# Performance work log

Measured on AMD Instinct MI355X. Metric: run time of the kernel, lower is better.

The kernel has to match this reference:

```python
import jax, jax.numpy as jnp
import numpy as np

B, N, C, H = 8, 1024, 768, 12
D = C // H  # head_dim = 64
SCALE = D ** -0.5
EPS = 1e-5  # nn.LayerNorm default


def layer_norm(x, gamma, beta):
    # normalize over last dim (head_dim)
    mu = jnp.mean(x, axis=-1, keepdims=True)
    var = jnp.var(x, axis=-1, keepdims=True)
    return (x - mu) * jax.lax.rsqrt(var + EPS) * gamma + beta


def setup_inputs() -> dict:
    key = jax.random.key(0)
    ks = jax.random.split(key, 5)
    s = 0.02
    return {
        "x": jax.random.normal(ks[0], (B, N, C), jnp.float32),
        "qkv_w": jax.random.normal(ks[1], (3 * C, C), jnp.float32) * s,
        "qkv_b": jax.random.normal(ks[2], (3 * C,), jnp.float32) * s,
        "q_gamma": jnp.ones((D,), jnp.float32),
        "q_beta": jnp.zeros((D,), jnp.float32),
        "k_gamma": jnp.ones((D,), jnp.float32),
        "k_beta": jnp.zeros((D,), jnp.float32),
        "proj_w": jax.random.normal(ks[3], (C, C), jnp.float32) * s,
        "proj_b": jax.random.normal(ks[4], (C,), jnp.float32) * s,
    }


def reference(x, qkv_w, qkv_b, q_gamma, q_beta, k_gamma, k_beta, proj_w, proj_b):
    Bx, Nx, Cx = x.shape
    qkv = x @ qkv_w.T + qkv_b                       # [B,N,3C]
    qkv = qkv.reshape(Bx, Nx, 3, H, D).transpose(2, 0, 3, 1, 4)  # [3,B,H,N,D]
    q, k, v = qkv[0], qkv[1], qkv[2]
    q = layer_norm(q, q_gamma, q_beta) * SCALE
    k = layer_norm(k, k_gamma, k_beta)
    attn = jax.nn.softmax(jnp.einsum('bhnd,bhmd->bhnm', q, k), axis=-1)  # [B,H,N,N]
    # attn_drop is identity (p=0, eval)
    out = jnp.einsum('bhnm,bhmd->bhnd', attn, v)    # [B,H,N,D]
    out = out.transpose(0, 2, 1, 3).reshape(Bx, Nx, Cx)
    out = out @ proj_w.T + proj_b                   # proj_drop identity
    return out, attn
```

## Files before the change

### kernel.cpp

```cpp
#include <hip/hip_runtime.h>
#include <hip/hip_bf16.h>
#include <stdint.h>

typedef __bf16 bf16_t;
typedef __bf16 bf16x8 __attribute__((ext_vector_type(8)));
typedef __bf16 bf16x4 __attribute__((ext_vector_type(4)));
typedef float f32x4 __attribute__((ext_vector_type(4)));

#define DEV static __device__ __forceinline__

DEV f32x4 mfma16(bf16x8 a, bf16x8 b, f32x4 c) {
  return __builtin_amdgcn_mfma_f32_16x16x32_bf16(a, b, c, 0, 0, 0);
}

DEV void gll16(const void* g, void* l) {
  __builtin_amdgcn_global_load_lds(
      (const __attribute__((address_space(1))) uint32_t*)g,
      (__attribute__((address_space(3))) uint32_t*)l, 16, 0, 0);
}

DEV int swz128(int row, int c16) {
  return (row << 7) + (((c16 ^ row) & 7) << 4);
}
DEV int swzel128(int row, int col) {
  return (row << 7) + ((((col >> 3) ^ row) & 7) << 4) + ((col & 7) << 1);
}

DEV void stage_tile_gll(const bf16_t* g, long rstride, char* lds, int wave, int lane) {
  int r0 = wave * 8 + (lane >> 3);
  int b = lane & 7;
#pragma unroll
  for (int q = 0; q < 2; q++) {
    int row = q * 32 + r0;
    gll16(g + (long)row * rstride + (((b ^ row) & 7) << 3),
          lds + q * 4096 + wave * 1024);
  }
}

__global__ void __launch_bounds__(256)
cast_all(const float* __restrict__ x, bf16_t* __restrict__ ox,
         const float* __restrict__ w1, bf16_t* __restrict__ ow1,
         const float* __restrict__ w2, bf16_t* __restrict__ ow2) {
  long i = (long)(blockIdx.x * 256 + threadIdx.x) * 8;
  const float* s; bf16_t* d; long off;
  if (i < 6291456L)      { s = x;  d = ox;  off = i; }
  else if (i < 8060928L) { s = w1; d = ow1; off = i - 6291456L; }
  else if (i < 8650752L) { s = w2; d = ow2; off = i - 8060928L; }
  else return;
  float4 a = *(const float4*)(s + off);
  float4 b = *(const float4*)(s + off + 4);
  bf16x8 v;
  v[0] = (bf16_t)a.x; v[1] = (bf16_t)a.y; v[2] = (bf16_t)a.z; v[3] = (bf16_t)a.w;
  v[4] = (bf16_t)b.x; v[5] = (bf16_t)b.y; v[6] = (bf16_t)b.z; v[7] = (bf16_t)b.w;
  *(bf16x8*)(d + off) = v;
}

#define C1Q 0.1803368801111244f

__global__ void __launch_bounds__(256, 2)
gemm_qkv_ln(const bf16_t* __restrict__ A, const bf16_t* __restrict__ Bw,
            const float* __restrict__ bias,
            const float* __restrict__ qg, const float* __restrict__ qb,
            const float* __restrict__ kg, const float* __restrict__ kb,
            bf16_t* __restrict__ qkv, int M, int N, int K) {
  __shared__ __align__(16) char As[8192];
  __shared__ __align__(16) char Bs[8192];
  const int tid = threadIdx.x;
  const int lane = tid & 63;
  const int wave = tid >> 6;
  const int wr = wave >> 1, wc = wave & 1;
  const int tileM = blockIdx.y << 7;
  const int tileN = blockIdx.x << 7;
  const int lrow = lane & 15, lk = lane >> 4;

  f32x4 acc[4][4];
  f32x4 z = {0.f, 0.f, 0.f, 0.f};
#pragma unroll
  for (int m = 0; m < 4; m++)
#pragma unroll
    for (int n = 0; n < 4; n++) acc[m][n] = z;

  const int srow = wave * 16 + (lane >> 2);
  const int sb = lane & 3;
  const bf16_t* Asrc0 = A + (long)(tileM + srow) * K + sb * 8;
  const bf16_t* Asrc1 = A + (long)(tileM + 64 + srow) * K + sb * 8;
  const bf16_t* Bsrc0 = Bw + (long)(tileN + srow) * K + sb * 8;
  const bf16_t* Bsrc1 = Bw + (long)(tileN + 64 + srow) * K + sb * 8;
  char* Adst = As + wave * 1024;
  char* Bdst = Bs + wave * 1024;

  for (int k0 = 0; k0 < K; k0 += 32) {
    __syncthreads();
    gll16(Asrc0 + k0, Adst);
    gll16(Asrc1 + k0, Adst + 4096);
    gll16(Bsrc0 + k0, Bdst);
    gll16(Bsrc1 + k0, Bdst + 4096);
    __syncthreads();
    bf16x8 af[4], bfr[4];
#pragma unroll
    for (int m = 0; m < 4; m++)
      af[m] = *(const bf16x8*)(As + (wr * 64 + m * 16 + lrow) * 64 + lk * 16);
#pragma unroll
    for (int n = 0; n < 4; n++)
      bfr[n] = *(const bf16x8*)(Bs + (wc * 64 + n * 16 + lrow) * 64 + lk * 16);
#pragma unroll
    for (int m = 0; m < 4; m++)
#pragma unroll
      for (int n = 0; n < 4; n++)
        acc[m][n] = mfma16(af[m], bfr[n], acc[m][n]);
  }

  const int t = tileN / 768;
  const int cbase = tileN + wc * 64;
  float g[4], be[4], bv[4];
#pragma unroll
  for (int n = 0; n < 4; n++) bv[n] = bias[cbase + n * 16 + lrow];
  if (t == 0) {
#pragma unroll
    for (int n = 0; n < 4; n++) {
      int d = n * 16 + lrow;
      g[n] = qg[d] * C1Q; be[n] = qb[d] * C1Q;
    }
  } else if (t == 1) {
#pragma unroll
    for (int n = 0; n < 4; n++) {
      int d = n * 16 + lrow;
      g[n] = kg[d]; be[n] = kb[d];
    }
  }

#pragma unroll
  for (int m = 0; m < 4; m++) {
#pragma unroll
    for (int r = 0; r < 4; r++) {
      float v[4];
#pragma unroll
      for (int n = 0; n < 4; n++) v[n] = acc[m][n][r] + bv[n];
      long row = tileM + wr * 64 + m * 16 + lk * 4 + r;
      bf16_t* dst = qkv + row * 2304 + cbase;
      if (t < 2) {
        float s = v[0] + v[1] + v[2] + v[3];
        float s2 = v[0]*v[0] + v[1]*v[1] + v[2]*v[2] + v[3]*v[3];
#pragma unroll
        for (int ofs = 1; ofs <= 8; ofs <<= 1) {
          s  += __shfl_xor(s, ofs);
          s2 += __shfl_xor(s2, ofs);
        }
        float mu = s * (1.f / 64.f);
        float rstd = rsqrtf(s2 * (1.f / 64.f) - mu * mu + 1e-5f);
#pragma unroll
        for (int n = 0; n < 4; n++)
          dst[n * 16 + lrow] = (bf16_t)((v[n] - mu) * rstd * g[n] + be[n]);
      } else {
#pragma unroll
        for (int n = 0; n < 4; n++)
          dst[n * 16 + lrow] = (bf16_t)v[n];
      }
    }
  }
}

__global__ void __launch_bounds__(256, 2)
gemm_bt(const bf16_t* __restrict__ A, const bf16_t* __restrict__ Bw,
        const float* __restrict__ bias, float* __restrict__ Cout,
        int M, int N, int K) {
  __shared__ __align__(16) char As[8192];
  __shared__ __align__(16) char Bs[8192];
  const int tid = threadIdx.x;
  const int lane = tid & 63;
  const int wave = tid >> 6;
  const int wr = wave >> 1, wc = wave & 1;
  const int tileM = blockIdx.y << 7;
  const int tileN = blockIdx.x << 7;
  const int lrow = lane & 15, lk = lane >> 4;

  f32x4 acc[4][4];
  f32x4 z = {0.f, 0.f, 0.f, 0.f};
#pragma unroll
  for (int m = 0; m < 4; m++)
#pragma unroll
    for (int n = 0; n < 4; n++) acc[m][n] = z;

  const int srow = wave * 16 + (lane >> 2);
  const int sb = lane & 3;
  const bf16_t* Asrc0 = A + (long)(tileM + srow) * K + sb * 8;
  const bf16_t* Asrc1 = A + (long)(tileM + 64 + srow) * K + sb * 8;
  const bf16_t* Bsrc0 = Bw + (long)(tileN + srow) * K + sb * 8;
  const bf16_t* Bsrc1 = Bw + (long)(tileN + 64 + srow) * K + sb * 8;
  char* Adst = As + wave * 1024;
  char* Bdst = Bs + wave * 1024;

  for (int k0 = 0; k0 < K; k0 += 32) {
    __syncthreads();
    gll16(Asrc0 + k0, Adst);
    gll16(Asrc1 + k0, Adst + 4096);
    gll16(Bsrc0 + k0, Bdst);
    gll16(Bsrc1 + k0, Bdst + 4096);
    __syncthreads();
    bf16x8 af[4], bfr[4];
#pragma unroll
    for (int m = 0; m < 4; m++)
      af[m] = *(const bf16x8*)(As + (wr * 64 + m * 16 + lrow) * 64 + lk * 16);
#pragma unroll
    for (int n = 0; n < 4; n++)
      bfr[n] = *(const bf16x8*)(Bs + (wc * 64 + n * 16 + lrow) * 64 + lk * 16);
#pragma unroll
    for (int m = 0; m < 4; m++)
#pragma unroll
      for (int n = 0; n < 4; n++)
        acc[m][n] = mfma16(af[m], bfr[n], acc[m][n]);
  }

  const int rg = lk;
#pragma unroll
  for (int n = 0; n < 4; n++) {
    int col = tileN + wc * 64 + n * 16 + lrow;
    float bv = bias[col];
#pragma unroll
    for (int m = 0; m < 4; m++) {
      long row0 = tileM + wr * 64 + m * 16 + rg * 4;
#pragma unroll
      for (int r = 0; r < 4; r++)
        Cout[(row0 + r) * N + col] = acc[m][n][r] + bv;
    }
  }
}

__global__ void __launch_bounds__(256, 2)
attn_kernel(const bf16_t* __restrict__ qkv, float* __restrict__ attn_out,
            bf16_t* __restrict__ out_heads) {
  const int tid = threadIdx.x;
  const int lane = tid & 63;
  const int wave = tid >> 6;
  const int lb = blockIdx.x;
  const int sid = (lb & 7) * 192 + (lb >> 3);
  const int qt = sid & 15;
  const int bh = sid >> 4;
  const int b = bh / 12, h = bh - b * 12;

  const bf16_t* base = qkv + (long)b * 2359296L + h * 64;
  const bf16_t* Qg = base;
  const bf16_t* Kg = base + 768;
  const bf16_t* Vg = base + 1536;

  __shared__ __align__(16) char Ks[16384];
  __shared__ __align__(16) char Vt[8192];
  __shared__ __align__(16) char QP[8192];

  const int lrow = lane & 15;
  const int lk = lane >> 4;

  stage_tile_gll(Qg + (long)(qt * 64) * 2304, 2304, QP, wave, lane);
  stage_tile_gll(Kg, 2304, Ks, wave, lane);
  __syncthreads();

  bf16x8 qf[2];
  qf[0] = *(const bf16x8*)(QP + swz128(wave * 16 + lrow, lk));
  qf[1] = *(const bf16x8*)(QP + swz128(wave * 16 + lrow, 4 + lk));

  auto computeS = [&](const char* Kb, f32x4 sfr[4]) {
    f32x4 z = {0.f, 0.f, 0.f, 0.f};
    sfr[0] = z; sfr[1] = z; sfr[2] = z; sfr[3] = z;
#pragma unroll
    for (int kk = 0; kk < 2; kk++)
#pragma unroll
      for (int f = 0; f < 4; f++) {
        bf16x8 kf = *(const bf16x8*)(Kb + swz128(f * 16 + lrow, kk * 4 + lk));
        sfr[f] = mfma16(qf[kk], kf, sfr[f]);
      }
  };

  float l_r[4] = {0.f, 0.f, 0.f, 0.f};

  for (int kt = 0; kt < 16; kt++) {
    if (kt < 15)
      stage_tile_gll(Kg + (long)((kt + 1) * 64) * 2304, 2304,
                     Ks + ((kt + 1) & 1) * 8192, wave, lane);
    f32x4 sfr[4];
    computeS(Ks + (kt & 1) * 8192, sfr);
#pragma unroll
    for (int r = 0; r < 4; r++)
      l_r[r] += exp2f(sfr[0][r]) + exp2f(sfr[1][r]) +
                exp2f(sfr[2][r]) + exp2f(sfr[3][r]);
    __syncthreads();
  }

  float il[4];
#pragma unroll
  for (int r = 0; r < 4; r++) {
#pragma unroll
    for (int ofs = 1; ofs <= 8; ofs <<= 1)
      l_r[r] += __shfl_xor(l_r[r], ofs);
    il[r] = 1.0f / l_r[r];
  }

  f32x4 of[4];
  {
    f32x4 z = {0.f, 0.f, 0.f, 0.f};
    of[0] = z; of[1] = z; of[2] = z; of[3] = z;
  }
  char* Pw = QP + wave * 2048;
  float* attn_base = attn_out + (long)bh * 1048576 + ((long)(qt * 64) << 10);

  stage_tile_gll(Kg, 2304, Ks, wave, lane);
  const int vk = lane, vdg = wave;
  bf16x8 vr0 = *(const bf16x8*)(Vg + (long)vk * 2304 + vdg * 16);
  bf16x8 vr1 = *(const bf16x8*)(Vg + (long)vk * 2304 + vdg * 16 + 8);

  for (int kt = 0; kt < 16; kt++) {
    __syncthreads();
#pragma unroll
    for (int j = 0; j < 8; j++) {
      *(bf16_t*)(Vt + swzel128(vdg * 16 + j, vk)) = vr0[j];
      *(bf16_t*)(Vt + swzel128(vdg * 16 + 8 + j, vk)) = vr1[j];
    }
    f32x4 sfr[4];
    computeS(Ks + (kt & 1) * 8192, sfr);
#pragma unroll
    for (int f = 0; f < 4; f++)
#pragma unroll
      for (int r = 0; r < 4; r++) {
        float p = exp2f(sfr[f][r]) * il[r];
        *(bf16_t*)(Pw + swzel128(lk * 4 + r, f * 16 + lrow)) = (bf16_t)p;
      }
    __syncthreads();
    if (kt < 15) {
      stage_tile_gll(Kg + (long)((kt + 1) * 64) * 2304, 2304,
                     Ks + ((kt + 1) & 1) * 8192, wave, lane);
      const bf16_t* vp = Vg + (long)((kt + 1) * 64 + vk) * 2304 + vdg * 16;
      vr0 = *(const bf16x8*)(vp);
      vr1 = *(const bf16x8*)(vp + 8);
    }
#pragma unroll
    for (int kk = 0; kk < 2; kk++) {
      bf16x8 pf = *(const bf16x8*)(Pw + swz128(lrow, kk * 4 + lk));
#pragma unroll
      for (int f = 0; f < 4; f++) {
        bf16x8 vf = *(const bf16x8*)(Vt + swz128(f * 16 + lrow, kk * 4 + lk));
        of[f] = mfma16(pf, vf, of[f]);
      }
    }
    float* ab = attn_base + kt * 64;
    {
      const int rsub = lane >> 4;
      const int c8 = lane & 15;
      const char* psrc = Pw + (c8 & 1) * 8;
#pragma unroll
      for (int i = 0; i < 4; i++) {
        int rl = i * 4 + rsub;
        bf16x4 pv = *(const bf16x4*)(psrc + swz128(rl, c8 >> 1));
        f32x4 v = {(float)pv[0], (float)pv[1], (float)pv[2], (float)pv[3]};
        __builtin_nontemporal_store(
            v, (f32x4*)(ab + ((long)(wave * 16 + rl) << 10) + c8 * 4));
      }
    }
  }

#pragma unroll
  for (int f = 0; f < 4; f++)
#pragma unroll
    for (int r = 0; r < 4; r++) {
      int nrow = qt * 64 + wave * 16 + lk * 4 + r;
      int d = f * 16 + lrow;
      out_heads[((long)b * 1024 + nrow) * 768 + h * 64 + d] = (bf16_t)of[f][r];
    }
}

extern "C" void kernel_launch(void* const* d_in, const int* in_sizes, int n_in,
                              void* d_out, int out_size, void* d_ws, size_t ws_size,
                              hipStream_t stream) {
  (void)in_sizes; (void)n_in; (void)out_size; (void)ws_size;
  const float* x       = (const float*)d_in[0];
  const float* qkv_w   = (const float*)d_in[1];
  const float* qkv_b   = (const float*)d_in[2];
  const float* q_gamma = (const float*)d_in[3];
  const float* q_beta  = (const float*)d_in[4];
  const float* k_gamma = (const float*)d_in[5];
  const float* k_beta  = (const float*)d_in[6];
  const float* proj_w  = (const float*)d_in[7];
  const float* proj_b  = (const float*)d_in[8];
  float* out = (float*)d_out;

  char* ws = (char*)d_ws;
  bf16_t* x_bf      = (bf16_t*)(ws);
  bf16_t* wqkv      = (bf16_t*)(ws + 12582912L);
  bf16_t* wproj     = (bf16_t*)(ws + 16121856L);
  bf16_t* qkv       = (bf16_t*)(ws + 17301504L);
  bf16_t* out_heads = (bf16_t*)(ws + 55050240L);

  cast_all<<<4224, 256, 0, stream>>>(x, x_bf, qkv_w, wqkv, proj_w, wproj);
  gemm_qkv_ln<<<dim3(18, 64), 256, 0, stream>>>(x_bf, wqkv, qkv_b,
                                                q_gamma, q_beta, k_gamma, k_beta,
                                                qkv, 8192, 2304, 768);
  attn_kernel<<<1536, 256, 0, stream>>>(qkv, out + 6291456L, out_heads);
  gemm_bt<<<dim3(6, 64), 256, 0, stream>>>(out_heads, wproj, proj_b, out, 8192, 768, 768);
}
```

Baseline: 190.5 us.

## Replace global_load_lds K staging with register-prefetched loads and LDS reuse

Removes the direct global-to-LDS async staging of Q and K tiles. Tiles are now loaded into registers a step ahead and written to LDS after the current tile's compute. This lets the K buffer shrink to one tile, with Vt used as the second K buffer during the normalizer pass, which cuts LDS per block and may raise occupancy. The cost is more VGPR pressure, an extra barrier per iteration in the second pass, and the loss of the asynchronous LDS fill.

```diff
diff --git a/kernel.cpp b/kernel.cpp
--- a/kernel.cpp
+++ b/kernel.cpp
@@ -24,17 +24,6 @@
 }
 DEV int swzel128(int row, int col) {
   return (row << 7) + ((((col >> 3) ^ row) & 7) << 4) + ((col & 7) << 1);
-}
-
-DEV void stage_tile_gll(const bf16_t* g, long rstride, char* lds, int wave, int lane) {
-  int r0 = wave * 8 + (lane >> 3);
-  int b = lane & 7;
-#pragma unroll
-  for (int q = 0; q < 2; q++) {
-    int row = q * 32 + r0;
-    gll16(g + (long)row * rstride + (((b ^ row) & 7) << 3),
-          lds + q * 4096 + wave * 1024);
-  }
 }
 
 __global__ void __launch_bounds__(256)
@@ -243,15 +232,27 @@
   const bf16_t* Kg = base + 768;
   const bf16_t* Vg = base + 1536;
 
-  __shared__ __align__(16) char Ks[16384];
+  __shared__ __align__(16) char Ks[8192];
   __shared__ __align__(16) char Vt[8192];
   __shared__ __align__(16) char QP[8192];
 
   const int lrow = lane & 15;
   const int lk = lane >> 4;
-
-  stage_tile_gll(Qg + (long)(qt * 64) * 2304, 2304, QP, wave, lane);
-  stage_tile_gll(Kg, 2304, Ks, wave, lane);
+  const int sr = tid >> 2;
+  const int sc = tid & 3;
+
+  {
+    const bf16_t* qp = Qg + (long)(qt * 64 + sr) * 2304 + sc * 8;
+    const bf16_t* kp = Kg + (long)sr * 2304 + sc * 8;
+    bf16x8 q0 = *(const bf16x8*)(qp);
+    bf16x8 q1 = *(const bf16x8*)(qp + 32);
+    bf16x8 k0 = *(const bf16x8*)(kp);
+    bf16x8 k1 = *(const bf16x8*)(kp + 32);
+    *(bf16x8*)(QP + swz128(sr, sc)) = q0;
+    *(bf16x8*)(QP + swz128(sr, 4 + sc)) = q1;
+    *(bf16x8*)(Ks + swz128(sr, sc)) = k0;
+    *(bf16x8*)(Ks + swz128(sr, 4 + sc)) = k1;
+  }
   __syncthreads();
 
   bf16x8 qf[2];
@@ -273,15 +274,24 @@
   float l_r[4] = {0.f, 0.f, 0.f, 0.f};
 
   for (int kt = 0; kt < 16; kt++) {
-    if (kt < 15)
-      stage_tile_gll(Kg + (long)((kt + 1) * 64) * 2304, 2304,
-                     Ks + ((kt + 1) & 1) * 8192, wave, lane);
+    const char* cur = (kt & 1) ? Vt : Ks;
+    bf16x8 kr0, kr1;
+    if (kt < 15) {
+      const bf16_t* kp = Kg + (long)((kt + 1) * 64 + sr) * 2304 + sc * 8;
+      kr0 = *(const bf16x8*)(kp);
+      kr1 = *(const bf16x8*)(kp + 32);
+    }
     f32x4 sfr[4];
-    computeS(Ks + (kt & 1) * 8192, sfr);
+    computeS(cur, sfr);
 #pragma unroll
     for (int r = 0; r < 4; r++)
       l_r[r] += exp2f(sfr[0][r]) + exp2f(sfr[1][r]) +
                 exp2f(sfr[2][r]) + exp2f(sfr[3][r]);
+    if (kt < 15) {
+      char* nxt = (kt & 1) ? Ks : Vt;
+      *(bf16x8*)(nxt + swz128(sr, sc)) = kr0;
+      *(bf16x8*)(nxt + swz128(sr, 4 + sc)) = kr1;
+    }
     __syncthreads();
   }
 
@@ -302,20 +312,36 @@
   char* Pw = QP + wave * 2048;
   float* attn_base = attn_out + (long)bh * 1048576 + ((long)(qt * 64) << 10);
 
-  stage_tile_gll(Kg, 2304, Ks, wave, lane);
   const int vk = lane, vdg = wave;
-  bf16x8 vr0 = *(const bf16x8*)(Vg + (long)vk * 2304 + vdg * 16);
-  bf16x8 vr1 = *(const bf16x8*)(Vg + (long)vk * 2304 + vdg * 16 + 8);
+  {
+    const bf16_t* kp = Kg + (long)sr * 2304 + sc * 8;
+    bf16x8 k0 = *(const bf16x8*)(kp);
+    bf16x8 k1 = *(const bf16x8*)(kp + 32);
+    const bf16_t* vp = Vg + (long)vk * 2304 + vdg * 16;
+    bf16x8 v0 = *(const bf16x8*)(vp);
+    bf16x8 v1 = *(const bf16x8*)(vp + 8);
+    *(bf16x8*)(Ks + swz128(sr, sc)) = k0;
+    *(bf16x8*)(Ks + swz128(sr, 4 + sc)) = k1;
+#pragma unroll
+    for (int j = 0; j < 8; j++) {
+      *(bf16_t*)(Vt + swzel128(vdg * 16 + j, vk)) = v0[j];
+      *(bf16_t*)(Vt + swzel128(vdg * 16 + 8 + j, vk)) = v1[j];
+    }
+  }
+  __syncthreads();
 
   for (int kt = 0; kt < 16; kt++) {
-    __syncthreads();
-#pragma unroll
-    for (int j = 0; j < 8; j++) {
-      *(bf16_t*)(Vt + swzel128(vdg * 16 + j, vk)) = vr0[j];
-      *(bf16_t*)(Vt + swzel128(vdg * 16 + 8 + j, vk)) = vr1[j];
+    bf16x8 kr0, kr1, vr0, vr1;
+    if (kt < 15) {
+      const bf16_t* kp = Kg + (long)((kt + 1) * 64 + sr) * 2304 + sc * 8;
+      kr0 = *(const bf16x8*)(kp);
+      kr1 = *(const bf16x8*)(kp + 32);
+      const bf16_t* vp = Vg + (long)((kt + 1) * 64 + vk) * 2304 + vdg * 16;
+      vr0 = *(const bf16x8*)(vp);
+      vr1 = *(const bf16x8*)(vp + 8);
     }
     f32x4 sfr[4];
-    computeS(Ks + (kt & 1) * 8192, sfr);
+    computeS(Ks, sfr);
 #pragma unroll
     for (int f = 0; f < 4; f++)
 #pragma unroll
@@ -323,14 +349,6 @@
         float p = exp2f(sfr[f][r]) * il[r];
         *(bf16_t*)(Pw + swzel128(lk * 4 + r, f * 16 + lrow)) = (bf16_t)p;
       }
-    __syncthreads();
-    if (kt < 15) {
-      stage_tile_gll(Kg + (long)((kt + 1) * 64) * 2304, 2304,
-                     Ks + ((kt + 1) & 1) * 8192, wave, lane);
-      const bf16_t* vp = Vg + (long)((kt + 1) * 64 + vk) * 2304 + vdg * 16;
-      vr0 = *(const bf16x8*)(vp);
-      vr1 = *(const bf16x8*)(vp + 8);
-    }
 #pragma unroll
     for (int kk = 0; kk < 2; kk++) {
       bf16x8 pf = *(const bf16x8*)(Pw + swz128(lrow, kk * 4 + lk));
@@ -354,6 +372,17 @@
             v, (f32x4*)(ab + ((long)(wave * 16 + rl) << 10) + c8 * 4));
       }
     }
+    __syncthreads();
+    if (kt < 15) {
+      *(bf16x8*)(Ks + swz128(sr, sc)) = kr0;
+      *(bf16x8*)(Ks + swz128(sr, 4 + sc)) = kr1;
+#pragma unroll
+      for (int j = 0; j < 8; j++) {
+        *(bf16_t*)(Vt + swzel128(vdg * 16 + j, vk)) = vr0[j];
+        *(bf16_t*)(Vt + swzel128(vdg * 16 + 8 + j, vk)) = vr1[j];
+      }
+    }
+    __syncthreads();
   }
 
 #pragma unroll
```

Result: no change. 189.0 us (-0.8%).
